# Kernel optimization log

Hardware: AMD Instinct MI355X
Metric: run time of the kernel (lower is better)

Reference implementation:

```python
import jax, jax.numpy as jnp
import numpy as np

# Cayley-Dickson octonion multiplication tables (from the source module)
SIGN_TABLE = np.array([
    [+1, -1, -1, -1, -1, -1, -1, -1],
    [+1, +1, +1, -1, +1, -1, -1, +1],
    [+1, -1, +1, +1, +1, +1, -1, -1],
    [+1, +1, -1, +1, +1, -1, +1, -1],
    [+1, -1, -1, -1, +1, +1, +1, +1],
    [+1, +1, -1, +1, -1, +1, -1, +1],
    [+1, +1, +1, -1, -1, +1, +1, -1],
    [+1, -1, +1, +1, -1, -1, +1, +1],
], dtype=np.float32)
WEIGHT_IDX = np.array([
    [0, 1, 2, 3, 4, 5, 6, 7],
    [1, 0, 3, 2, 5, 4, 7, 6],
    [2, 3, 0, 1, 6, 7, 4, 5],
    [3, 2, 1, 0, 7, 6, 5, 4],
    [4, 5, 6, 7, 0, 1, 2, 3],
    [5, 4, 7, 6, 1, 0, 3, 2],
    [6, 7, 4, 5, 2, 3, 0, 1],
    [7, 6, 5, 4, 3, 2, 1, 0],
], dtype=np.int32)

B, T, D_IN, D_OUT = 4, 2048, 4096, 4096
K = D_IN // 8   # per-component input dim
N = D_OUT // 8  # per-component output dim


def setup_inputs() -> dict:
    key = jax.random.key(0)
    k1, k2 = jax.random.split(key)
    x = jax.random.normal(k1, (B, T, D_IN), dtype=jnp.float32)
    weight = jax.random.normal(k2, (8, N, K), dtype=jnp.float32) * (1.0 / np.sqrt(K))
    return {"x": x, "weight": weight}


def reference(x, weight):
    """Fused octonion (Cayley-Dickson) linear layer.

    y_i = sum_j sign[i,j] * x_j @ W[widx[i,j]].T
    x components are contiguous chunks of the last dim: x_j = x[..., j*K:(j+1)*K].
    """
    b, t, f = x.shape
    k = f // 8
    xs = x.reshape(b, t, 8, k)                 # [B,T,8,K], component axis j
    Wg = weight[jnp.asarray(WEIGHT_IDX)]        # [8(i),8(j),N,K] gathered weights
    S = jnp.asarray(SIGN_TABLE, dtype=x.dtype)  # [8(i),8(j)]
    # contract over j (component) and k (features); produce [B,T,i,N]
    y = jnp.einsum('ij,btjk,ijnk->btin', S, xs, Wg)
    return y.reshape(b, t, -1)                  # [B,T,8*N]
```

## Files before the change

kernel.cpp:

```cpp
#include <hip/hip_runtime.h>
#include <stdint.h>

typedef __attribute__((ext_vector_type(8))) short bf16x8;
typedef __attribute__((ext_vector_type(4))) float f32x4;

#define D_IN  4096
#define D_OUT 4096
#define KC 512
#define NC 512
#define NT 64

__constant__ float c_sign[64] = {
 +1,-1,-1,-1,-1,-1,-1,-1,
 +1,+1,+1,-1,+1,-1,-1,+1,
 +1,-1,+1,+1,+1,+1,-1,-1,
 +1,+1,-1,+1,+1,-1,+1,-1,
 +1,-1,-1,-1,+1,+1,+1,+1,
 +1,+1,-1,+1,-1,+1,-1,+1,
 +1,+1,+1,-1,-1,+1,+1,-1,
 +1,-1,+1,+1,-1,-1,+1,+1,
};

__device__ inline unsigned int pack2bf16(float a, float b) {
    unsigned int ua = __builtin_bit_cast(unsigned int, a);
    unsigned int ub = __builtin_bit_cast(unsigned int, b);
    ua = (ua + 0x7FFFu + ((ua >> 16) & 1u)) >> 16;
    ub = (ub + 0x7FFFu + ((ub >> 16) & 1u)) >> 16;
    return ua | (ub << 16);
}

typedef __attribute__((address_space(1))) const unsigned int gas_u32;
typedef __attribute__((address_space(3))) unsigned int las_u32;
#define ASYNC16(g, l) __builtin_amdgcn_global_load_lds((gas_u32*)(g), (las_u32*)(l), 16, 0, 0)


__global__ __launch_bounds__(256)
void conv_x(const float* __restrict__ in, unsigned short* __restrict__ out, int n8) {
    int i = blockIdx.x * blockDim.x + threadIdx.x;
    if (i >= n8) return;
    const float4 a = ((const float4*)in)[(size_t)i * 2];
    const float4 b = ((const float4*)in)[(size_t)i * 2 + 1];
    uint4 o;
    o.x = pack2bf16(a.x, a.y); o.y = pack2bf16(a.z, a.w);
    o.z = pack2bf16(b.x, b.y); o.w = pack2bf16(b.z, b.w);
    ((uint4*)out)[i] = o;
}

__global__ __launch_bounds__(256)
void conv_w(const float* __restrict__ W, unsigned short* __restrict__ out) {
    int gid = blockIdx.x * blockDim.x + threadIdx.x;
    int row = gid >> 9;
    int c8  = gid & 511;
    int i = row >> 9, n = row & 511;
    int j = c8 >> 6;
    int k = (c8 & 63) << 3;
    float sgn = c_sign[i * 8 + j];
    const float* src = W + ((((i ^ j) * NC + n) * KC) + k);
    float4 a = *(const float4*)(src);
    float4 b = *(const float4*)(src + 4);
    uint4 o;
    o.x = pack2bf16(a.x * sgn, a.y * sgn); o.y = pack2bf16(a.z * sgn, a.w * sgn);
    o.z = pack2bf16(b.x * sgn, b.y * sgn); o.w = pack2bf16(b.z * sgn, b.w * sgn);
    ((uint4*)out)[gid] = o;
}


template<int P>
__device__ __forceinline__ void do_phase(
    const unsigned short* bufA, const unsigned short* bufB,
    f32x4 (&acc)[8][4], bf16x8 (&bfr)[4][2],
    const unsigned short* stg_g, unsigned short* stg_l,
    size_t goff0, size_t goff1, int loff0, int loff1,
    int lane, int wr, int wc)
{
    bf16x8 afr[2][2];
    #pragma unroll
    for (int q = 0; q < 2; ++q) {
        const int r = wr * 128 + (2 * P + q) * 16 + (lane & 15);
        #pragma unroll
        for (int kk = 0; kk < 2; ++kk) {
            const int ch = (kk * 4 + (lane >> 4)) ^ (r & 7);
            afr[q][kk] = *(const bf16x8*)((const char*)bufA + r * 128 + ch * 16);
        }
    }
    if (P == 0) {
        #pragma unroll
        for (int n = 0; n < 4; ++n) {
            const int r = wc * 64 + n * 16 + (lane & 15);
            #pragma unroll
            for (int kk = 0; kk < 2; ++kk) {
                const int ch = (kk * 4 + (lane >> 4)) ^ (r & 7);
                bfr[n][kk] = *(const bf16x8*)((const char*)bufB + r * 128 + ch * 16);
            }
        }
    }
    ASYNC16(stg_g + goff0, stg_l + loff0);
    ASYNC16(stg_g + goff1, stg_l + loff1);
    __builtin_amdgcn_s_barrier();
    asm volatile("s_waitcnt lgkmcnt(0)");
    __builtin_amdgcn_s_setprio(1);
    #pragma unroll
    for (int kk = 0; kk < 2; ++kk)
        #pragma unroll
        for (int q = 0; q < 2; ++q)
            #pragma unroll
            for (int n = 0; n < 4; ++n)
                acc[2 * P + q][n] = __builtin_amdgcn_mfma_f32_16x16x32_bf16(
                    afr[q][kk], bfr[n][kk], acc[2 * P + q][n], 0, 0, 0);
    __builtin_amdgcn_s_setprio(0);
}

#define ENDP do { __builtin_amdgcn_s_barrier(); asm volatile("" ::: "memory"); } while (0)

__global__ __launch_bounds__(512, 2)
void octo_gemm_8ph(const unsigned short* __restrict__ Xb,
                   const unsigned short* __restrict__ Wb,
                   float* __restrict__ Y, int M)
{
    __shared__ __align__(16) unsigned short sm[65536];
    unsigned short* A0 = sm;
    unsigned short* A1 = sm + 16384;
    unsigned short* B0 = sm + 32768;
    unsigned short* B1 = sm + 49152;

    const int tid  = threadIdx.x;
    const int lane = tid & 63;
    const int wave = tid >> 6;
    const int wr   = wave >> 2;
    const int wc   = wave & 3;

    const int nbn = D_OUT / 256;
    const int nwg = (M / 256) * nbn;
    int bid = blockIdx.x;
    int cpx = nwg >> 3;
    int wg  = (bid & 7) * cpx + (bid >> 3);
    const int bm = wg / nbn, bn = wg % nbn;
    const int row0 = bm * 256, col0 = bn * 256;

    const int srow  = tid >> 3;
    const int sch   = tid & 7;
    const size_t goff0 = (size_t)srow * D_IN + (size_t)((sch ^ (srow & 7)) * 8);
    const size_t goff1 = goff0 + (size_t)64 * D_IN;
    const int loff0 = tid * 8;
    const int loff1 = loff0 + 4096;

    const unsigned short* gX = Xb + (size_t)row0 * D_IN;
    const unsigned short* gW = Wb + (size_t)col0 * D_IN;

    f32x4 acc[8][4];
    #pragma unroll
    for (int m = 0; m < 8; ++m)
        #pragma unroll
        for (int n = 0; n < 4; ++n)
            acc[m][n] = (f32x4){0.f, 0.f, 0.f, 0.f};

    ASYNC16(gX + goff0, A0 + loff0);              ASYNC16(gX + goff1, A0 + loff1);
    ASYNC16(gX + 128 * D_IN + goff0, A0 + 8192 + loff0);
    ASYNC16(gX + 128 * D_IN + goff1, A0 + 8192 + loff1);
    ASYNC16(gW + goff0, B0 + loff0);              ASYNC16(gW + goff1, B0 + loff1);
    ASYNC16(gW + 128 * D_IN + goff0, B0 + 8192 + loff0);
    ASYNC16(gW + 128 * D_IN + goff1, B0 + 8192 + loff1);
    ASYNC16(gW + 64 + goff0, B1 + loff0);         ASYNC16(gW + 64 + goff1, B1 + loff1);
    ASYNC16(gW + 64 + 128 * D_IN + goff0, B1 + 8192 + loff0);
    ASYNC16(gW + 64 + 128 * D_IN + goff1, B1 + 8192 + loff1);
    asm volatile("s_waitcnt vmcnt(4)");
    ENDP;

    bf16x8 bfr[4][2];
    for (int i = 0; i < NT / 2; ++i) {
        const int u = 2 * i;
        const unsigned short* gA1t = gX + ((u + 1) & (NT - 1)) * 64;
        const unsigned short* gA2t = gX + ((u + 2) & (NT - 1)) * 64;
        const unsigned short* gB2t = gW + ((u + 2) & (NT - 1)) * 64;
        const unsigned short* gB3t = gW + ((u + 3) & (NT - 1)) * 64;

        do_phase<0>(A0, B0, acc, bfr, gA1t,            A1,        goff0, goff1, loff0, loff1, lane, wr, wc);
        ENDP;
        do_phase<1>(A0, B0, acc, bfr, gA1t + 128*D_IN, A1 + 8192, goff0, goff1, loff0, loff1, lane, wr, wc);
        ENDP;
        do_phase<2>(A0, B0, acc, bfr, gB2t,            B0,        goff0, goff1, loff0, loff1, lane, wr, wc);
        ENDP;
        do_phase<3>(A0, B0, acc, bfr, gB2t + 128*D_IN, B0 + 8192, goff0, goff1, loff0, loff1, lane, wr, wc);
        asm volatile("s_waitcnt vmcnt(4)");
        ENDP;
        do_phase<0>(A1, B1, acc, bfr, gA2t,            A0,        goff0, goff1, loff0, loff1, lane, wr, wc);
        ENDP;
        do_phase<1>(A1, B1, acc, bfr, gA2t + 128*D_IN, A0 + 8192, goff0, goff1, loff0, loff1, lane, wr, wc);
        ENDP;
        do_phase<2>(A1, B1, acc, bfr, gB3t,            B1,        goff0, goff1, loff0, loff1, lane, wr, wc);
        ENDP;
        do_phase<3>(A1, B1, acc, bfr, gB3t + 128*D_IN, B1 + 8192, goff0, goff1, loff0, loff1, lane, wr, wc);
        asm volatile("s_waitcnt vmcnt(4)");
        ENDP;
    }

    const int rl = (lane >> 4) << 2;
    const int cl = lane & 15;
    #pragma unroll
    for (int m = 0; m < 8; ++m) {
        const int rg = row0 + wr * 128 + m * 16 + rl;
        #pragma unroll
        for (int n = 0; n < 4; ++n) {
            const int cg = col0 + wc * 64 + n * 16 + cl;
            #pragma unroll
            for (int q = 0; q < 4; ++q)
                Y[(size_t)(rg + q) * D_OUT + cg] = acc[m][n][q];
        }
    }
}


#define BM 128
#define BN 128
#define BK 64

__global__ __launch_bounds__(256)
void octo_gemm_f32(const float* __restrict__ X, const float* __restrict__ W,
                   float* __restrict__ Y, int M)
{
    __shared__ __align__(16) unsigned short As[BM * BK];
    __shared__ __align__(16) unsigned short Bs[BN * BK];

    const int tid  = threadIdx.x;
    const int lane = tid & 63;
    const int wave = tid >> 6;
    const int wr   = wave >> 1;
    const int wc   = wave & 1;

    const int nbn = D_OUT / BN;
    const int nwg = (M / BM) * nbn;
    int bid = blockIdx.x;
    int wg  = bid;
    if ((nwg & 7) == 0) {
        int cpx = nwg >> 3;
        wg = (bid & 7) * cpx + (bid >> 3);
    }
    const int bm = wg / nbn, bn = wg % nbn;
    const int row0  = bm * BM;
    const int col0  = bn * BN;
    const int icomp = col0 >> 9;
    const int noff  = col0 & (NC - 1);

    const int srow = tid >> 4;
    const int scol = (tid & 15) << 2;

    f32x4 acc[4][4];
    #pragma unroll
    for (int m = 0; m < 4; ++m)
        #pragma unroll
        for (int n = 0; n < 4; ++n)
            acc[m][n] = (f32x4){0.f, 0.f, 0.f, 0.f};

    char* AsB = (char*)As;
    char* BsB = (char*)Bs;
    const int byteC = scol << 1;

    for (int step = 0; step < NT; ++step) {
        const int k0 = step * BK;
        const int j  = k0 >> 9;
        const int kc = k0 & (KC - 1);
        const float sgn = c_sign[icomp * 8 + j];
        const int   w   = icomp ^ j;
        const float* Wp = W + (((size_t)w * NC + noff) * KC + kc);
        const float* Xp = X + ((size_t)row0 * D_IN + k0);

        __syncthreads();
        #pragma unroll
        for (int p = 0; p < 8; ++p) {
            const int r  = p * 16 + srow;
            const int sb = r * 128 + ((((byteC >> 4) ^ (r & 7)) << 4)) + (byteC & 8);
            const float4 va = *(const float4*)(&Xp[(size_t)r * D_IN + scol]);
            *(uint2*)(AsB + sb) = make_uint2(pack2bf16(va.x, va.y),
                                             pack2bf16(va.z, va.w));
            const float4 vb = *(const float4*)(&Wp[(size_t)r * KC + scol]);
            *(uint2*)(BsB + sb) = make_uint2(pack2bf16(vb.x * sgn, vb.y * sgn),
                                             pack2bf16(vb.z * sgn, vb.w * sgn));
        }
        __syncthreads();

        #pragma unroll
        for (int kk = 0; kk < 2; ++kk) {
            bf16x8 af[4], bf[4];
            #pragma unroll
            for (int m = 0; m < 4; ++m) {
                const int r = wr * 64 + m * 16 + (lane & 15);
                const int chunk = (kk * 4 + (lane >> 4)) ^ (r & 7);
                af[m] = *(const bf16x8*)(AsB + r * 128 + (chunk << 4));
            }
            #pragma unroll
            for (int n = 0; n < 4; ++n) {
                const int r = wc * 64 + n * 16 + (lane & 15);
                const int chunk = (kk * 4 + (lane >> 4)) ^ (r & 7);
                bf[n] = *(const bf16x8*)(BsB + r * 128 + (chunk << 4));
            }
            #pragma unroll
            for (int m = 0; m < 4; ++m)
                #pragma unroll
                for (int n = 0; n < 4; ++n)
                    acc[m][n] = __builtin_amdgcn_mfma_f32_16x16x32_bf16(
                        af[m], bf[n], acc[m][n], 0, 0, 0);
        }
    }

    const int rl = (lane >> 4) << 2;
    const int cl = lane & 15;
    #pragma unroll
    for (int m = 0; m < 4; ++m) {
        const int rg = row0 + wr * 64 + m * 16 + rl;
        #pragma unroll
        for (int n = 0; n < 4; ++n) {
            const int cg = col0 + wc * 64 + n * 16 + cl;
            #pragma unroll
            for (int q = 0; q < 4; ++q)
                Y[(size_t)(rg + q) * D_OUT + cg] = acc[m][n][q];
        }
    }
}

extern "C" void kernel_launch(void* const* d_in, const int* in_sizes, int n_in,
                              void* d_out, int out_size, void* d_ws, size_t ws_size,
                              hipStream_t stream) {
    const float* X = (const float*)d_in[0];
    const float* W = (const float*)d_in[1];
    float* Y = (float*)d_out;
    const int M = in_sizes[0] / D_IN;

    const size_t xb_bytes = (size_t)M * D_IN * sizeof(unsigned short);
    const size_t wb_bytes = (size_t)D_OUT * D_IN * sizeof(unsigned short);

    if (ws_size >= xb_bytes + wb_bytes && (M % 256) == 0) {
        unsigned short* Xb = (unsigned short*)d_ws;
        unsigned short* Wb = (unsigned short*)((char*)d_ws + xb_bytes);
        const int n8x = M * D_IN / 8;
        hipLaunchKernelGGL(conv_x, dim3(n8x / 256), dim3(256), 0, stream, X, Xb, n8x);
        hipLaunchKernelGGL(conv_w, dim3((D_OUT * D_IN / 8) / 256), dim3(256), 0, stream, W, Wb);
        const int nwg = (M / 256) * (D_OUT / 256);
        hipLaunchKernelGGL(octo_gemm_8ph, dim3(nwg), dim3(512), 0, stream, Xb, Wb, Y, M);
    } else {
        const int nwg = (M / BM) * (D_OUT / BN);
        hipLaunchKernelGGL(octo_gemm_f32, dim3(nwg), dim3(256), 0, stream, X, W, Y, M);
    }
}
```

Measured before the change: 263.5 us.

## Reorder k-tile phases to software-pipeline LDS fragment reads under MFMAs

Restructures each k-tile's four phases so each phase handles one k-half and one M-half. The next phase's A fragments are read from LDS right after the current MFMA batch, and B fragments for both k-halves are loaded once up front. The explicit lgkmcnt(0) wait is dropped, leaving the compiler to place LDS waits so reads can overlap matrix work. This raises register pressure from extra live fragments and changes the barrier and async-copy interleaving, which could affect occupancy at two blocks per CU.

```diff
diff --git a/kernel.cpp b/kernel.cpp
--- a/kernel.cpp
+++ b/kernel.cpp
@@ -65,52 +65,79 @@
 }
 
 
-template<int P>
-__device__ __forceinline__ void do_phase(
-    const unsigned short* bufA, const unsigned short* bufB,
-    f32x4 (&acc)[8][4], bf16x8 (&bfr)[4][2],
-    const unsigned short* stg_g, unsigned short* stg_l,
+#define ENDP do { __builtin_amdgcn_s_barrier(); asm volatile("" ::: "memory"); } while (0)
+
+__device__ __forceinline__ void read_a(bf16x8 (&d)[4], const unsigned short* buf,
+                                       int mh, int kk, int lane, int wr) {
+#pragma unroll
+    for (int f = 0; f < 4; ++f) {
+        const int r  = wr * 128 + (mh * 4 + f) * 16 + (lane & 15);
+        const int ch = (kk * 4 + (lane >> 4)) ^ (r & 7);
+        d[f] = *(const bf16x8*)((const char*)buf + r * 128 + (ch << 4));
+    }
+}
+
+__device__ __forceinline__ void read_b(bf16x8 (&d)[4], const unsigned short* buf,
+                                       int kk, int lane, int wc) {
+#pragma unroll
+    for (int n = 0; n < 4; ++n) {
+        const int r  = wc * 64 + n * 16 + (lane & 15);
+        const int ch = (kk * 4 + (lane >> 4)) ^ (r & 7);
+        d[n] = *(const bf16x8*)((const char*)buf + r * 128 + (ch << 4));
+    }
+}
+
+__device__ __forceinline__ void mfma8(f32x4 (&acc)[8][4], int mh,
+                                      const bf16x8 (&a)[4], const bf16x8 (&b)[4]) {
+#pragma unroll
+    for (int f = 0; f < 4; ++f)
+#pragma unroll
+        for (int n = 0; n < 4; ++n)
+            acc[mh * 4 + f][n] = __builtin_amdgcn_mfma_f32_16x16x32_bf16(
+                a[f], b[n], acc[mh * 4 + f][n], 0, 0, 0);
+}
+
+__device__ __forceinline__ void ktile(
+    const unsigned short* Abuf, const unsigned short* Bbuf,
+    f32x4 (&acc)[8][4],
+    const unsigned short* sg0, unsigned short* sl0,
+    const unsigned short* sg1, unsigned short* sl1,
+    const unsigned short* sg2, unsigned short* sl2,
+    const unsigned short* sg3, unsigned short* sl3,
     size_t goff0, size_t goff1, int loff0, int loff1,
     int lane, int wr, int wc)
 {
-    bf16x8 afr[2][2];
-    #pragma unroll
-    for (int q = 0; q < 2; ++q) {
-        const int r = wr * 128 + (2 * P + q) * 16 + (lane & 15);
-        #pragma unroll
-        for (int kk = 0; kk < 2; ++kk) {
-            const int ch = (kk * 4 + (lane >> 4)) ^ (r & 7);
-            afr[q][kk] = *(const bf16x8*)((const char*)bufA + r * 128 + ch * 16);
-        }
-    }
-    if (P == 0) {
-        #pragma unroll
-        for (int n = 0; n < 4; ++n) {
-            const int r = wc * 64 + n * 16 + (lane & 15);
-            #pragma unroll
-            for (int kk = 0; kk < 2; ++kk) {
-                const int ch = (kk * 4 + (lane >> 4)) ^ (r & 7);
-                bfr[n][kk] = *(const bf16x8*)((const char*)bufB + r * 128 + ch * 16);
-            }
-        }
-    }
-    ASYNC16(stg_g + goff0, stg_l + loff0);
-    ASYNC16(stg_g + goff1, stg_l + loff1);
+    bf16x8 a0[4], a1[4], b0[4], b1[4];
+    read_a(a0, Abuf, 0, 0, lane, wr);
+    read_b(b0, Bbuf, 0, lane, wc);
+    read_b(b1, Bbuf, 1, lane, wc);
+    ASYNC16(sg0 + goff0, sl0 + loff0); ASYNC16(sg0 + goff1, sl0 + loff1);
     __builtin_amdgcn_s_barrier();
-    asm volatile("s_waitcnt lgkmcnt(0)");
     __builtin_amdgcn_s_setprio(1);
-    #pragma unroll
-    for (int kk = 0; kk < 2; ++kk)
-        #pragma unroll
-        for (int q = 0; q < 2; ++q)
-            #pragma unroll
-            for (int n = 0; n < 4; ++n)
-                acc[2 * P + q][n] = __builtin_amdgcn_mfma_f32_16x16x32_bf16(
-                    afr[q][kk], bfr[n][kk], acc[2 * P + q][n], 0, 0, 0);
+    mfma8(acc, 0, a0, b0);
     __builtin_amdgcn_s_setprio(0);
-}
-
-#define ENDP do { __builtin_amdgcn_s_barrier(); asm volatile("" ::: "memory"); } while (0)
+    read_a(a1, Abuf, 1, 0, lane, wr);
+    ENDP;
+    ASYNC16(sg1 + goff0, sl1 + loff0); ASYNC16(sg1 + goff1, sl1 + loff1);
+    __builtin_amdgcn_s_barrier();
+    __builtin_amdgcn_s_setprio(1);
+    mfma8(acc, 1, a1, b0);
+    __builtin_amdgcn_s_setprio(0);
+    read_a(a0, Abuf, 0, 1, lane, wr);
+    ENDP;
+    ASYNC16(sg2 + goff0, sl2 + loff0); ASYNC16(sg2 + goff1, sl2 + loff1);
+    __builtin_amdgcn_s_barrier();
+    __builtin_amdgcn_s_setprio(1);
+    mfma8(acc, 0, a0, b1);
+    __builtin_amdgcn_s_setprio(0);
+    read_a(a1, Abuf, 1, 1, lane, wr);
+    ENDP;
+    ASYNC16(sg3 + goff0, sl3 + loff0); ASYNC16(sg3 + goff1, sl3 + loff1);
+    __builtin_amdgcn_s_barrier();
+    __builtin_amdgcn_s_setprio(1);
+    mfma8(acc, 1, a1, b1);
+    __builtin_amdgcn_s_setprio(0);
+}
 
 __global__ __launch_bounds__(512, 2)
 void octo_gemm_8ph(const unsigned short* __restrict__ Xb,
@@ -166,7 +193,6 @@
     asm volatile("s_waitcnt vmcnt(4)");
     ENDP;
 
-    bf16x8 bfr[4][2];
     for (int i = 0; i < NT / 2; ++i) {
         const int u = 2 * i;
         const unsigned short* gA1t = gX + ((u + 1) & (NT - 1)) * 64;
@@ -174,22 +200,20 @@
         const unsigned short* gB2t = gW + ((u + 2) & (NT - 1)) * 64;
         const unsigned short* gB3t = gW + ((u + 3) & (NT - 1)) * 64;
 
-        do_phase<0>(A0, B0, acc, bfr, gA1t,            A1,        goff0, goff1, loff0, loff1, lane, wr, wc);
-        ENDP;
-        do_phase<1>(A0, B0, acc, bfr, gA1t + 128*D_IN, A1 + 8192, goff0, goff1, loff0, loff1, lane, wr, wc);
-        ENDP;
-        do_phase<2>(A0, B0, acc, bfr, gB2t,            B0,        goff0, goff1, loff0, loff1, lane, wr, wc);
-        ENDP;
-        do_phase<3>(A0, B0, acc, bfr, gB2t + 128*D_IN, B0 + 8192, goff0, goff1, loff0, loff1, lane, wr, wc);
+        ktile(A0, B0, acc,
+              gA1t,              A1,
+              gA1t + 128 * D_IN, A1 + 8192,
+              gB2t,              B0,
+              gB2t + 128 * D_IN, B0 + 8192,
+              goff0, goff1, loff0, loff1, lane, wr, wc);
         asm volatile("s_waitcnt vmcnt(4)");
         ENDP;
-        do_phase<0>(A1, B1, acc, bfr, gA2t,            A0,        goff0, goff1, loff0, loff1, lane, wr, wc);
-        ENDP;
-        do_phase<1>(A1, B1, acc, bfr, gA2t + 128*D_IN, A0 + 8192, goff0, goff1, loff0, loff1, lane, wr, wc);
-        ENDP;
-        do_phase<2>(A1, B1, acc, bfr, gB3t,            B1,        goff0, goff1, loff0, loff1, lane, wr, wc);
-        ENDP;
-        do_phase<3>(A1, B1, acc, bfr, gB3t + 128*D_IN, B1 + 8192, goff0, goff1, loff0, loff1, lane, wr, wc);
+        ktile(A1, B1, acc,
+              gA2t,              A0,
+              gA2t + 128 * D_IN, A0 + 8192,
+              gB3t,              B1,
+              gB3t + 128 * D_IN, B1 + 8192,
+              goff0, goff1, loff0, loff1, lane, wr, wc);
         asm volatile("s_waitcnt vmcnt(4)");
         ENDP;
     }
```

After: 263.3 us. About the same (-0.1%).
